# Kernel tuning notes

Measured on AMD Instinct MI355X. Metric: run time of the kernel, lower is better.

The kernel has to match this reference:

```python
import jax, jax.numpy as jnp
import numpy as np

N_NODES = 100000
N_EDGES = 3200000
IN_F = 128
HID = 32


def setup_inputs() -> dict:
    key = jax.random.key(0)
    k = jax.random.split(key, 8)
    x = jax.random.normal(k[0], (N_NODES, IN_F), dtype=jnp.float32)
    edge_index = jax.random.randint(k[1], (2, N_EDGES), 0, N_NODES, dtype=jnp.int64)
    edge_weight = jax.random.uniform(k[2], (N_EDGES,), dtype=jnp.float32)
    # GCN conv weight (in -> 32) and bias, then Linear(32 -> 1)
    s1 = 1.0 / np.sqrt(IN_F)
    s2 = 1.0 / np.sqrt(HID)
    W1 = jax.random.uniform(k[3], (IN_F, HID), dtype=jnp.float32, minval=-s1, maxval=s1)
    b1 = jax.random.uniform(k[4], (HID,), dtype=jnp.float32, minval=-s1, maxval=s1)
    W2 = jax.random.uniform(k[5], (HID, 1), dtype=jnp.float32, minval=-s2, maxval=s2)
    b2 = jax.random.uniform(k[6], (1,), dtype=jnp.float32, minval=-s2, maxval=s2)
    return {"x": x, "edge_index": edge_index, "edge_weight": edge_weight,
            "W1": W1, "b1": b1, "W2": W2, "b2": b2}


def gcn_conv(x, edge_index, edge_weight, W, b):
    N = x.shape[0]
    src = edge_index[0]
    dst = edge_index[1]
    loop = jnp.arange(N, dtype=edge_index.dtype)
    row = jnp.concatenate([dst, loop])  # aggregation targets
    col = jnp.concatenate([src, loop])  # message sources
    w = jnp.concatenate([edge_weight, jnp.ones((N,), dtype=x.dtype)])
    deg = jax.ops.segment_sum(w, row, num_segments=N)
    dinv = jnp.where(deg > 0, deg ** -0.5, 0.0).astype(x.dtype)
    norm = dinv[row] * w * dinv[col]  # [E+N]
    h = x @ W  # [N, 32]  transform before gather (cheaper)
    msgs = norm[:, None] * h[col]  # [E+N, 32]
    agg = jax.ops.segment_sum(msgs, row, num_segments=N)  # [N, 32]
    return agg + b


def reference(x, edge_index, edge_weight, W1, b1, W2, b2):
    h = gcn_conv(x, edge_index, edge_weight, W1, b1)
    h = jax.nn.relu(h)
    return h @ W2 + b2  # [N, 1]
```

## Files before the change

kernel.cpp:

```cpp
#include <hip/hip_runtime.h>
#include <hip/hip_bf16.h>
#include <hip/hip_fp16.h>

#define NN 100000
#define NE 3200000
#define IN_F 128
#define HID 32

#define NB 782
#define NBP1 (NB + 1)
#define BNODES 128
#define PBLK 782
#define EPB 4096
#define SSPAN 4608

typedef __hip_bfloat16 bf16;
typedef __attribute__((ext_vector_type(8))) short s16x8;
typedef __attribute__((ext_vector_type(4))) float f32x4;

__global__ __launch_bounds__(512) void k_part(const int* __restrict__ ei,
                                              const float* __restrict__ ew,
                                              int* __restrict__ offs,
                                              uint2* __restrict__ raw) {
    __shared__ int hist[NB];
    __shared__ int start[NB];
    __shared__ int wtot8[8];
    __shared__ uint2 sp[EPB];

    int t = threadIdx.x;
    int blk = blockIdx.x;
    for (int b = t; b < NB; b += 512) hist[b] = 0;
    __syncthreads();

    unsigned pk[8]; unsigned wb[8]; int bkt[8];
    int base_e = blk * EPB;
#pragma unroll
    for (int j = 0; j < 8; j++) {
        int e = base_e + j * 512 + t;
        if (e < NE) {
            int src = __builtin_nontemporal_load(ei + e);
            int dst = __builtin_nontemporal_load(ei + NE + e);
            float w = __builtin_nontemporal_load(ew + e);
            bkt[j] = dst >> 7;
            pk[j] = (unsigned)src | ((unsigned)(dst & 127) << 20);
            wb[j] = __float_as_uint(w);
        } else bkt[j] = -1;
    }
#pragma unroll
    for (int j = 0; j < 8; j++)
        if (bkt[j] >= 0) atomicAdd(&hist[bkt[j]], 1);
    __syncthreads();

    int e0 = 2 * t, e1 = 2 * t + 1;
    int h0 = (e0 < NB) ? hist[e0] : 0;
    int h1 = (e1 < NB) ? hist[e1] : 0;
    int psum = h0 + h1;
    int lane = t & 63;
    int incl = psum;
#pragma unroll
    for (int off = 1; off < 64; off <<= 1) {
        int up = __shfl_up(incl, off, 64);
        if (lane >= off) incl += up;
    }
    int wid = t >> 6;
    if (lane == 63) wtot8[wid] = incl;
    __syncthreads();
    int woff = 0;
    for (int wj = 0; wj < wid; wj++) woff += wtot8[wj];
    int exc = woff + incl - psum;
    if (e0 < NB) start[e0] = exc;
    if (e1 < NB) start[e1] = exc + h0;
    __syncthreads();

    int total = start[NB - 1] + hist[NB - 1];
    int* orow = offs + (size_t)blk * NBP1;
    for (int b = t; b < NB; b += 512) orow[b] = start[b];
    if (t == 0) orow[NB] = total;
    __syncthreads();

#pragma unroll
    for (int j = 0; j < 8; j++) {
        if (bkt[j] >= 0) {
            int pos = atomicAdd(&start[bkt[j]], 1);
            sp[pos] = make_uint2(pk[j], wb[j]);
        }
    }
    __syncthreads();

    uint2* r = raw + (size_t)blk * EPB;
    for (int i = t; i < total; i += 512) r[i] = sp[i];
}

__global__ __launch_bounds__(256) void k_trans(const int* __restrict__ in, int* __restrict__ out) {
    __shared__ int tile[32][33];
    int c0 = blockIdx.x * 32, r0 = blockIdx.y * 32;
    int tx = threadIdx.x & 31, ty = threadIdx.x >> 5;
    for (int i = ty; i < 32; i += 8) {
        int r = r0 + i, c = c0 + tx;
        if (r < PBLK && c < NBP1) tile[i][tx] = in[(size_t)r * NBP1 + c];
    }
    __syncthreads();
    for (int i = ty; i < 32; i += 8) {
        int c = c0 + i, r = r0 + tx;
        if (c < NBP1 && r < PBLK) out[(size_t)c * PBLK + r] = tile[tx][i];
    }
}

__global__ __launch_bounds__(512) void k_sort(const int* __restrict__ offsT,
                                              const uint2* __restrict__ raw,
                                              uint2* __restrict__ srt,
                                              int* __restrict__ rowstart,
                                              int* __restrict__ rowcnt,
                                              float* __restrict__ dinv) {
    __shared__ uint2 se[SSPAN];
    __shared__ unsigned short runid[SSPAN];
    __shared__ int P[PBLK + 1];
    __shared__ int O0[PBLK];
    __shared__ int hist[BNODES];
    __shared__ float wsum[BNODES];
    __shared__ int scanbuf[BNODES];
    __shared__ int cur[BNODES];
    __shared__ int wt8[8];

    int t = threadIdx.x;
    int b = blockIdx.x;
    if (t < BNODES) { hist[t] = 0; wsum[t] = 1.0f; }

    int e0 = 2 * t, e1 = 2 * t + 1;
    int l0 = 0, l1 = 0, o0v = 0, o1v = 0;
    if (e0 < PBLK) {
        o0v = offsT[(size_t)b * PBLK + e0];
        l0  = offsT[(size_t)(b + 1) * PBLK + e0] - o0v;
    }
    if (e1 < PBLK) {
        o1v = offsT[(size_t)b * PBLK + e1];
        l1  = offsT[(size_t)(b + 1) * PBLK + e1] - o1v;
    }
    int psum = l0 + l1;
    int lane = t & 63;
    int incl = psum;
#pragma unroll
    for (int off = 1; off < 64; off <<= 1) {
        int up = __shfl_up(incl, off, 64);
        if (lane >= off) incl += up;
    }
    int wid = t >> 6;
    if (lane == 63) wt8[wid] = incl;
    __syncthreads();
    int woff = 0;
    for (int wj = 0; wj < wid; wj++) woff += wt8[wj];
    int exc = woff + incl - psum;
    if (e0 < PBLK) { P[e0] = exc;      O0[e0] = o0v; }
    if (e1 < PBLK) { P[e1] = exc + l0; O0[e1] = o1v; }
    if (t == 0) {
        int s = 0;
#pragma unroll
        for (int j = 0; j < 8; j++) s += wt8[j];
        P[PBLK] = s;
    }
    __syncthreads();

    int total = min(P[PBLK], SSPAN);

    for (int r = t; r < PBLK; r += 512) {
        int p0 = P[r], p1 = min(P[r + 1], SSPAN);
        for (int i = p0; i < p1; i++) runid[i] = (unsigned short)r;
    }
    __syncthreads();

    uint2 rr[9];
#pragma unroll
    for (int k = 0; k < 9; k++) {
        int d = t + k * 512;
        if (d < total) {
            int r = runid[d];
            uint2 rec = raw[(size_t)r * EPB + O0[r] + (d - P[r])];
            rr[k] = rec;
            int dl = (rec.x >> 20) & 127;
            atomicAdd(&hist[dl], 1);
            atomicAdd(&wsum[dl], __uint_as_float(rec.y));
        }
    }
    __syncthreads();

    if (t < BNODES) scanbuf[t] = hist[t];
    __syncthreads();
    for (int off = 1; off < BNODES; off <<= 1) {
        int v = 0;
        if (t < BNODES && t >= off) v = scanbuf[t - off];
        __syncthreads();
        if (t < BNODES) scanbuf[t] += v;
        __syncthreads();
    }

    int obase = b * SSPAN;
    if (t < BNODES) {
        int binstart = scanbuf[t] - hist[t];
        cur[t] = binstart;
        int node = b * BNODES + t;
        if (node < NN) {
            rowstart[node] = obase + binstart;
            rowcnt[node]   = hist[t];
            dinv[node]     = rsqrtf(wsum[t]);
        }
    }
    __syncthreads();

#pragma unroll
    for (int k = 0; k < 9; k++) {
        int d = t + k * 512;
        if (d < total) {
            uint2 rec = rr[k];
            int dl = (rec.x >> 20) & 127;
            int pos = atomicAdd(&cur[dl], 1);
            se[pos] = make_uint2(rec.x & 0xFFFFF, rec.y);
        }
    }
    __syncthreads();

    for (int i = t; i < total; i += 512) srt[obase + i] = se[i];
}

__global__ void k_w1frag(const float* __restrict__ W1, unsigned short* __restrict__ wfrag) {
    int lane = threadIdx.x;
    int q = lane >> 4;
    int n0 = lane & 15;
#pragma unroll
    for (int ks = 0; ks < 4; ks++) {
#pragma unroll
        for (int nt = 0; nt < 2; nt++) {
            int fi = ks * 2 + nt;
            int n = n0 + 16 * nt;
#pragma unroll
            for (int j = 0; j < 8; j++) {
                int k = ks * 32 + q * 8 + j;
                float v = W1[k * HID + n];
                __hip_bfloat16 bv = __float2bfloat16(v);
                wfrag[((size_t)fi * 64 + lane) * 8 + j] = *(unsigned short*)&bv;
            }
        }
    }
}

__global__ __launch_bounds__(256) void k_hs(const float* __restrict__ x,
                                            const unsigned short* __restrict__ wfrag,
                                            const float* __restrict__ dinv,
                                            bf16* __restrict__ hs) {
    int t = threadIdx.x;
    int lane = t & 63;
    int wv = t >> 6;
    int base = blockIdx.x * 64 + wv * 16;
    int m = lane & 15;
    int q = lane >> 4;
    int node = base + m;

    s16x8 wf[8];
    const s16x8* wp = (const s16x8*)wfrag;
#pragma unroll
    for (int fi = 0; fi < 8; fi++) wf[fi] = wp[fi * 64 + lane];

    f32x4 acc0 = {0.f, 0.f, 0.f, 0.f};
    f32x4 acc1 = {0.f, 0.f, 0.f, 0.f};

    const float* rowp = x + (size_t)node * IN_F + q * 8;
    bool valid = (node < NN);

#pragma unroll
    for (int ks = 0; ks < 4; ks++) {
        float4 f0 = {0,0,0,0}, f1 = {0,0,0,0};
        if (valid) {
            const float4* xr = (const float4*)(rowp + ks * 32);
            f0 = xr[0]; f1 = xr[1];
        }
        union { s16x8 v; unsigned u32[4]; } af;
        __hip_bfloat162 p0 = __float22bfloat162_rn({f0.x, f0.y});
        __hip_bfloat162 p1 = __float22bfloat162_rn({f0.z, f0.w});
        __hip_bfloat162 p2 = __float22bfloat162_rn({f1.x, f1.y});
        __hip_bfloat162 p3 = __float22bfloat162_rn({f1.z, f1.w});
        af.u32[0] = *(unsigned*)&p0;
        af.u32[1] = *(unsigned*)&p1;
        af.u32[2] = *(unsigned*)&p2;
        af.u32[3] = *(unsigned*)&p3;
        acc0 = __builtin_amdgcn_mfma_f32_16x16x32_bf16(af.v, wf[ks * 2 + 0], acc0, 0, 0, 0);
        acc1 = __builtin_amdgcn_mfma_f32_16x16x32_bf16(af.v, wf[ks * 2 + 1], acc1, 0, 0, 0);
    }

    int f = lane & 15;
#pragma unroll
    for (int r = 0; r < 4; r++) {
        int n2 = base + q * 4 + r;
        if (n2 < NN) {
            float dv = dinv[n2];
            hs[(size_t)n2 * HID + f]      = __float2bfloat16(dv * acc0[r]);
            hs[(size_t)n2 * HID + f + 16] = __float2bfloat16(dv * acc1[r]);
        }
    }
}

__global__ __launch_bounds__(256) void k_agg(const int* __restrict__ rowstart,
                                             const int* __restrict__ rowcnt,
                                             const uint2* __restrict__ eb,
                                             const bf16* __restrict__ hs,
                                             const float* __restrict__ dinv,
                                             const float* __restrict__ b1, const float* __restrict__ W2,
                                             const float* __restrict__ b2, float* __restrict__ out) {
    int t = threadIdx.x;
    int l = t & 15;
    int node = blockIdx.x * 16 + (t >> 4);
    int rs = rowstart[node];
    int re = rs + rowcnt[node];
    const __hip_bfloat162* hs2 = (const __hip_bfloat162*)hs;
    float acc0 = 0.f, acc1 = 0.f;

    for (int base = rs; base < re; base += 16) {
        int idx = base + l;
        int sreg = 0; float wreg = 0.f;
        if (idx < re) {
            uint2 r = eb[idx];
            sreg = (int)r.x;
            wreg = __uint_as_float(r.y);
        }
        int m = min(16, re - base);
        int j = 0;
        for (; j + 8 <= m; j += 8) {
            int s0 = __shfl(sreg, j + 0, 16), s1 = __shfl(sreg, j + 1, 16);
            int s2 = __shfl(sreg, j + 2, 16), s3 = __shfl(sreg, j + 3, 16);
            int s4 = __shfl(sreg, j + 4, 16), s5 = __shfl(sreg, j + 5, 16);
            int s6 = __shfl(sreg, j + 6, 16), s7 = __shfl(sreg, j + 7, 16);
            float w0 = __shfl(wreg, j + 0, 16), w1 = __shfl(wreg, j + 1, 16);
            float w2 = __shfl(wreg, j + 2, 16), w3 = __shfl(wreg, j + 3, 16);
            float w4 = __shfl(wreg, j + 4, 16), w5 = __shfl(wreg, j + 5, 16);
            float w6 = __shfl(wreg, j + 6, 16), w7 = __shfl(wreg, j + 7, 16);
            __hip_bfloat162 h0 = hs2[(size_t)s0 * 16 + l];
            __hip_bfloat162 h1 = hs2[(size_t)s1 * 16 + l];
            __hip_bfloat162 h2 = hs2[(size_t)s2 * 16 + l];
            __hip_bfloat162 h3 = hs2[(size_t)s3 * 16 + l];
            __hip_bfloat162 h4 = hs2[(size_t)s4 * 16 + l];
            __hip_bfloat162 h5 = hs2[(size_t)s5 * 16 + l];
            __hip_bfloat162 h6 = hs2[(size_t)s6 * 16 + l];
            __hip_bfloat162 h7 = hs2[(size_t)s7 * 16 + l];
            float2 f0 = __bfloat1622float2(h0); acc0 += w0 * f0.x; acc1 += w0 * f0.y;
            float2 f1 = __bfloat1622float2(h1); acc0 += w1 * f1.x; acc1 += w1 * f1.y;
            float2 f2 = __bfloat1622float2(h2); acc0 += w2 * f2.x; acc1 += w2 * f2.y;
            float2 f3 = __bfloat1622float2(h3); acc0 += w3 * f3.x; acc1 += w3 * f3.y;
            float2 f4 = __bfloat1622float2(h4); acc0 += w4 * f4.x; acc1 += w4 * f4.y;
            float2 f5 = __bfloat1622float2(h5); acc0 += w5 * f5.x; acc1 += w5 * f5.y;
            float2 f6 = __bfloat1622float2(h6); acc0 += w6 * f6.x; acc1 += w6 * f6.y;
            float2 f7 = __bfloat1622float2(h7); acc0 += w7 * f7.x; acc1 += w7 * f7.y;
        }
        for (; j < m; j++) {
            int s = __shfl(sreg, j, 16);
            float w = __shfl(wreg, j, 16);
            float2 fv = __bfloat1622float2(hs2[(size_t)s * 16 + l]);
            acc0 += w * fv.x; acc1 += w * fv.y;
        }
    }

    float2 fs = __bfloat1622float2(hs2[(size_t)node * 16 + l]);
    float dv = dinv[node];
    float v0 = dv * (acc0 + fs.x) + b1[2 * l];
    float v1 = dv * (acc1 + fs.y) + b1[2 * l + 1];
    v0 = fmaxf(v0, 0.f);
    v1 = fmaxf(v1, 0.f);
    float psum = v0 * W2[2 * l] + v1 * W2[2 * l + 1];
#pragma unroll
    for (int m2 = 8; m2 >= 1; m2 >>= 1) psum += __shfl_xor(psum, m2, 16);
    if (l == 0) out[node] = psum + b2[0];
}

extern "C" void kernel_launch(void* const* d_in, const int* in_sizes, int n_in,
                              void* d_out, int out_size, void* d_ws, size_t ws_size,
                              hipStream_t stream) {
    const float* x  = (const float*)d_in[0];
    const int*   ei = (const int*)d_in[1];
    const float* ew = (const float*)d_in[2];
    const float* W1 = (const float*)d_in[3];
    const float* b1 = (const float*)d_in[4];
    const float* W2 = (const float*)d_in[5];
    const float* b2 = (const float*)d_in[6];
    float* out = (float*)d_out;

    char* ws = (char*)d_ws;
    uint2*          raw      = (uint2*)         (ws + 0);
    bf16*           hs       = (bf16*)          (ws + 0);
    int*            offs     = (int*)           (ws + 25624576);
    int*            offsT    = (int*)           (ws + 28073984);
    uint2*          srt      = (uint2*)         (ws + 30523392);
    int*            rowstart = (int*)           (ws + 59351040);
    int*            rowcnt   = (int*)           (ws + 59751040);
    float*          dinv     = (float*)         (ws + 60151040);
    unsigned short* wfrag    = (unsigned short*)(ws + 60551040);

    k_w1frag<<<1, 64, 0, stream>>>(W1, wfrag);
    k_part<<<PBLK, 512, 0, stream>>>(ei, ew, offs, raw);
    k_trans<<<dim3((NBP1 + 31) / 32, (PBLK + 31) / 32), 256, 0, stream>>>(offs, offsT);
    k_sort<<<NB, 512, 0, stream>>>(offsT, raw, srt, rowstart, rowcnt, dinv);
    k_hs<<<(NN + 63) / 64, 256, 0, stream>>>(x, wfrag, dinv, hs);
    k_agg<<<NN / 16, 256, 0, stream>>>(rowstart, rowcnt, srt, hs, dinv, b1, W2, b2, out);
}
```

Before: 216.6 us.

## Fuse per-bucket sort into aggregation kernel and compute degrees via global fixed-point atomics

Removes the separate sort kernel. The bucket sort now runs in shared memory inside the aggregation kernel, so the sorted edge array no longer goes through global memory. Weighted degrees are accumulated during partitioning with integer atomics on a fixed-point scale into a zeroed global buffer, and dinv is derived in the hs kernel. This costs 3.2M global atomics, a memset, some fixed-point rounding in the degree, and a heavier aggregation kernel where each 16-lane group handles 4 nodes serially, with fewer blocks and lower occupancy.

```diff
diff --git a/kernel.cpp b/kernel.cpp
--- a/kernel.cpp
+++ b/kernel.cpp
@@ -13,6 +13,8 @@
 #define PBLK 782
 #define EPB 4096
 #define SSPAN 4608
+#define WSCALE 16777216.0f
+#define WSCALE_INV 5.9604644775390625e-08f
 
 typedef __hip_bfloat16 bf16;
 typedef __attribute__((ext_vector_type(8))) short s16x8;
@@ -21,7 +23,8 @@
 __global__ __launch_bounds__(512) void k_part(const int* __restrict__ ei,
                                               const float* __restrict__ ew,
                                               int* __restrict__ offs,
-                                              uint2* __restrict__ raw) {
+                                              uint2* __restrict__ raw,
+                                              int* __restrict__ wsumi) {
     __shared__ int hist[NB];
     __shared__ int start[NB];
     __shared__ int wtot8[8];
@@ -48,7 +51,11 @@
     }
 #pragma unroll
     for (int j = 0; j < 8; j++)
-        if (bkt[j] >= 0) atomicAdd(&hist[bkt[j]], 1);
+        if (bkt[j] >= 0) {
+            atomicAdd(&hist[bkt[j]], 1);
+            int dst = (bkt[j] << 7) | (int)((pk[j] >> 20) & 127);
+            atomicAdd(&wsumi[dst], (int)(__uint_as_float(wb[j]) * WSCALE));
+        }
     __syncthreads();
 
     int e0 = 2 * t, e1 = 2 * t + 1;
@@ -106,121 +113,6 @@
     }
 }
 
-__global__ __launch_bounds__(512) void k_sort(const int* __restrict__ offsT,
-                                              const uint2* __restrict__ raw,
-                                              uint2* __restrict__ srt,
-                                              int* __restrict__ rowstart,
-                                              int* __restrict__ rowcnt,
-                                              float* __restrict__ dinv) {
-    __shared__ uint2 se[SSPAN];
-    __shared__ unsigned short runid[SSPAN];
-    __shared__ int P[PBLK + 1];
-    __shared__ int O0[PBLK];
-    __shared__ int hist[BNODES];
-    __shared__ float wsum[BNODES];
-    __shared__ int scanbuf[BNODES];
-    __shared__ int cur[BNODES];
-    __shared__ int wt8[8];
-
-    int t = threadIdx.x;
-    int b = blockIdx.x;
-    if (t < BNODES) { hist[t] = 0; wsum[t] = 1.0f; }
-
-    int e0 = 2 * t, e1 = 2 * t + 1;
-    int l0 = 0, l1 = 0, o0v = 0, o1v = 0;
-    if (e0 < PBLK) {
-        o0v = offsT[(size_t)b * PBLK + e0];
-        l0  = offsT[(size_t)(b + 1) * PBLK + e0] - o0v;
-    }
-    if (e1 < PBLK) {
-        o1v = offsT[(size_t)b * PBLK + e1];
-        l1  = offsT[(size_t)(b + 1) * PBLK + e1] - o1v;
-    }
-    int psum = l0 + l1;
-    int lane = t & 63;
-    int incl = psum;
-#pragma unroll
-    for (int off = 1; off < 64; off <<= 1) {
-        int up = __shfl_up(incl, off, 64);
-        if (lane >= off) incl += up;
-    }
-    int wid = t >> 6;
-    if (lane == 63) wt8[wid] = incl;
-    __syncthreads();
-    int woff = 0;
-    for (int wj = 0; wj < wid; wj++) woff += wt8[wj];
-    int exc = woff + incl - psum;
-    if (e0 < PBLK) { P[e0] = exc;      O0[e0] = o0v; }
-    if (e1 < PBLK) { P[e1] = exc + l0; O0[e1] = o1v; }
-    if (t == 0) {
-        int s = 0;
-#pragma unroll
-        for (int j = 0; j < 8; j++) s += wt8[j];
-        P[PBLK] = s;
-    }
-    __syncthreads();
-
-    int total = min(P[PBLK], SSPAN);
-
-    for (int r = t; r < PBLK; r += 512) {
-        int p0 = P[r], p1 = min(P[r + 1], SSPAN);
-        for (int i = p0; i < p1; i++) runid[i] = (unsigned short)r;
-    }
-    __syncthreads();
-
-    uint2 rr[9];
-#pragma unroll
-    for (int k = 0; k < 9; k++) {
-        int d = t + k * 512;
-        if (d < total) {
-            int r = runid[d];
-            uint2 rec = raw[(size_t)r * EPB + O0[r] + (d - P[r])];
-            rr[k] = rec;
-            int dl = (rec.x >> 20) & 127;
-            atomicAdd(&hist[dl], 1);
-            atomicAdd(&wsum[dl], __uint_as_float(rec.y));
-        }
-    }
-    __syncthreads();
-
-    if (t < BNODES) scanbuf[t] = hist[t];
-    __syncthreads();
-    for (int off = 1; off < BNODES; off <<= 1) {
-        int v = 0;
-        if (t < BNODES && t >= off) v = scanbuf[t - off];
-        __syncthreads();
-        if (t < BNODES) scanbuf[t] += v;
-        __syncthreads();
-    }
-
-    int obase = b * SSPAN;
-    if (t < BNODES) {
-        int binstart = scanbuf[t] - hist[t];
-        cur[t] = binstart;
-        int node = b * BNODES + t;
-        if (node < NN) {
-            rowstart[node] = obase + binstart;
-            rowcnt[node]   = hist[t];
-            dinv[node]     = rsqrtf(wsum[t]);
-        }
-    }
-    __syncthreads();
-
-#pragma unroll
-    for (int k = 0; k < 9; k++) {
-        int d = t + k * 512;
-        if (d < total) {
-            uint2 rec = rr[k];
-            int dl = (rec.x >> 20) & 127;
-            int pos = atomicAdd(&cur[dl], 1);
-            se[pos] = make_uint2(rec.x & 0xFFFFF, rec.y);
-        }
-    }
-    __syncthreads();
-
-    for (int i = t; i < total; i += 512) srt[obase + i] = se[i];
-}
-
 __global__ void k_w1frag(const float* __restrict__ W1, unsigned short* __restrict__ wfrag) {
     int lane = threadIdx.x;
     int q = lane >> 4;
@@ -244,7 +136,8 @@
 
 __global__ __launch_bounds__(256) void k_hs(const float* __restrict__ x,
                                             const unsigned short* __restrict__ wfrag,
-                                            const float* __restrict__ dinv,
+                                            const int* __restrict__ wsumi,
+                                            float* __restrict__ dinv,
                                             bf16* __restrict__ hs) {
     int t = threadIdx.x;
     int lane = t & 63;
@@ -290,82 +183,172 @@
     for (int r = 0; r < 4; r++) {
         int n2 = base + q * 4 + r;
         if (n2 < NN) {
-            float dv = dinv[n2];
+            float dv = rsqrtf((float)wsumi[n2] * WSCALE_INV + 1.0f);
+            if (f == 0) dinv[n2] = dv;
             hs[(size_t)n2 * HID + f]      = __float2bfloat16(dv * acc0[r]);
             hs[(size_t)n2 * HID + f + 16] = __float2bfloat16(dv * acc1[r]);
         }
     }
 }
 
-__global__ __launch_bounds__(256) void k_agg(const int* __restrict__ rowstart,
-                                             const int* __restrict__ rowcnt,
-                                             const uint2* __restrict__ eb,
+__global__ __launch_bounds__(512) void k_agg(const int* __restrict__ offsT,
+                                             const uint2* __restrict__ raw,
                                              const bf16* __restrict__ hs,
                                              const float* __restrict__ dinv,
                                              const float* __restrict__ b1, const float* __restrict__ W2,
                                              const float* __restrict__ b2, float* __restrict__ out) {
+    __shared__ uint2 se[SSPAN];
+    __shared__ int P[PBLK + 1];
+    __shared__ int basearr[PBLK];
+    __shared__ int hist[BNODES];
+    __shared__ int scanbuf[BNODES];
+    __shared__ int cur[BNODES];
+    __shared__ int wt8[8];
+
+    unsigned short* runid = (unsigned short*)se;
+
     int t = threadIdx.x;
+    int b = blockIdx.x;
+    if (t < BNODES) hist[t] = 0;
+
+    int e0 = 2 * t, e1 = 2 * t + 1;
+    int l0 = 0, l1 = 0, o0v = 0, o1v = 0;
+    if (e0 < PBLK) {
+        o0v = offsT[(size_t)b * PBLK + e0];
+        l0  = offsT[(size_t)(b + 1) * PBLK + e0] - o0v;
+    }
+    if (e1 < PBLK) {
+        o1v = offsT[(size_t)b * PBLK + e1];
+        l1  = offsT[(size_t)(b + 1) * PBLK + e1] - o1v;
+    }
+    int psum = l0 + l1;
+    int lane = t & 63;
+    int incl = psum;
+#pragma unroll
+    for (int off = 1; off < 64; off <<= 1) {
+        int up = __shfl_up(incl, off, 64);
+        if (lane >= off) incl += up;
+    }
+    int wid = t >> 6;
+    if (lane == 63) wt8[wid] = incl;
+    __syncthreads();
+    int woff = 0;
+    for (int wj = 0; wj < wid; wj++) woff += wt8[wj];
+    int exc = woff + incl - psum;
+    if (e0 < PBLK) { P[e0] = exc;      basearr[e0] = o0v - exc; }
+    if (e1 < PBLK) { P[e1] = exc + l0; basearr[e1] = o1v - (exc + l0); }
+    if (t == 0) {
+        int s = 0;
+#pragma unroll
+        for (int j = 0; j < 8; j++) s += wt8[j];
+        P[PBLK] = s;
+    }
+    __syncthreads();
+
+    int total = min(P[PBLK], SSPAN);
+
+    for (int r = t; r < PBLK; r += 512) {
+        int p0 = P[r], p1 = min(P[r + 1], SSPAN);
+        for (int i = p0; i < p1; i++) runid[i] = (unsigned short)r;
+    }
+    __syncthreads();
+
+    uint2 rr[9];
+#pragma unroll
+    for (int k = 0; k < 9; k++) {
+        int d = t + k * 512;
+        if (d < total) {
+            int r = runid[d];
+            uint2 rec = raw[(size_t)r * EPB + (basearr[r] + d)];
+            rr[k] = rec;
+            int dl = (rec.x >> 20) & 127;
+            atomicAdd(&hist[dl], 1);
+        }
+    }
+    __syncthreads();
+
+    if (t < BNODES) scanbuf[t] = hist[t];
+    __syncthreads();
+    for (int off = 1; off < BNODES; off <<= 1) {
+        int v = 0;
+        if (t < BNODES && t >= off) v = scanbuf[t - off];
+        __syncthreads();
+        if (t < BNODES) scanbuf[t] += v;
+        __syncthreads();
+    }
+    if (t < BNODES) cur[t] = scanbuf[t] - hist[t];
+    __syncthreads();
+
+#pragma unroll
+    for (int k = 0; k < 9; k++) {
+        int d = t + k * 512;
+        if (d < total) {
+            uint2 rec = rr[k];
+            int dl = (rec.x >> 20) & 127;
+            int pos = atomicAdd(&cur[dl], 1);
+            se[pos] = make_uint2(rec.x & 0xFFFFF, rec.y);
+        }
+    }
+    __syncthreads();
+
+    int gid = t >> 4;
     int l = t & 15;
-    int node = blockIdx.x * 16 + (t >> 4);
-    int rs = rowstart[node];
-    int re = rs + rowcnt[node];
     const __hip_bfloat162* hs2 = (const __hip_bfloat162*)hs;
-    float acc0 = 0.f, acc1 = 0.f;
-
-    for (int base = rs; base < re; base += 16) {
-        int idx = base + l;
-        int sreg = 0; float wreg = 0.f;
-        if (idx < re) {
-            uint2 r = eb[idx];
-            sreg = (int)r.x;
-            wreg = __uint_as_float(r.y);
-        }
-        int m = min(16, re - base);
-        int j = 0;
-        for (; j + 8 <= m; j += 8) {
-            int s0 = __shfl(sreg, j + 0, 16), s1 = __shfl(sreg, j + 1, 16);
-            int s2 = __shfl(sreg, j + 2, 16), s3 = __shfl(sreg, j + 3, 16);
-            int s4 = __shfl(sreg, j + 4, 16), s5 = __shfl(sreg, j + 5, 16);
-            int s6 = __shfl(sreg, j + 6, 16), s7 = __shfl(sreg, j + 7, 16);
-            float w0 = __shfl(wreg, j + 0, 16), w1 = __shfl(wreg, j + 1, 16);
-            float w2 = __shfl(wreg, j + 2, 16), w3 = __shfl(wreg, j + 3, 16);
-            float w4 = __shfl(wreg, j + 4, 16), w5 = __shfl(wreg, j + 5, 16);
-            float w6 = __shfl(wreg, j + 6, 16), w7 = __shfl(wreg, j + 7, 16);
-            __hip_bfloat162 h0 = hs2[(size_t)s0 * 16 + l];
-            __hip_bfloat162 h1 = hs2[(size_t)s1 * 16 + l];
-            __hip_bfloat162 h2 = hs2[(size_t)s2 * 16 + l];
-            __hip_bfloat162 h3 = hs2[(size_t)s3 * 16 + l];
-            __hip_bfloat162 h4 = hs2[(size_t)s4 * 16 + l];
-            __hip_bfloat162 h5 = hs2[(size_t)s5 * 16 + l];
-            __hip_bfloat162 h6 = hs2[(size_t)s6 * 16 + l];
-            __hip_bfloat162 h7 = hs2[(size_t)s7 * 16 + l];
-            float2 f0 = __bfloat1622float2(h0); acc0 += w0 * f0.x; acc1 += w0 * f0.y;
-            float2 f1 = __bfloat1622float2(h1); acc0 += w1 * f1.x; acc1 += w1 * f1.y;
-            float2 f2 = __bfloat1622float2(h2); acc0 += w2 * f2.x; acc1 += w2 * f2.y;
-            float2 f3 = __bfloat1622float2(h3); acc0 += w3 * f3.x; acc1 += w3 * f3.y;
-            float2 f4 = __bfloat1622float2(h4); acc0 += w4 * f4.x; acc1 += w4 * f4.y;
-            float2 f5 = __bfloat1622float2(h5); acc0 += w5 * f5.x; acc1 += w5 * f5.y;
-            float2 f6 = __bfloat1622float2(h6); acc0 += w6 * f6.x; acc1 += w6 * f6.y;
-            float2 f7 = __bfloat1622float2(h7); acc0 += w7 * f7.x; acc1 += w7 * f7.y;
-        }
-        for (; j < m; j++) {
-            int s = __shfl(sreg, j, 16);
-            float w = __shfl(wreg, j, 16);
-            float2 fv = __bfloat1622float2(hs2[(size_t)s * 16 + l]);
-            acc0 += w * fv.x; acc1 += w * fv.y;
-        }
-    }
-
-    float2 fs = __bfloat1622float2(hs2[(size_t)node * 16 + l]);
-    float dv = dinv[node];
-    float v0 = dv * (acc0 + fs.x) + b1[2 * l];
-    float v1 = dv * (acc1 + fs.y) + b1[2 * l + 1];
-    v0 = fmaxf(v0, 0.f);
-    v1 = fmaxf(v1, 0.f);
-    float psum = v0 * W2[2 * l] + v1 * W2[2 * l + 1];
-#pragma unroll
-    for (int m2 = 8; m2 >= 1; m2 >>= 1) psum += __shfl_xor(psum, m2, 16);
-    if (l == 0) out[node] = psum + b2[0];
+#pragma unroll
+    for (int nn = 0; nn < 4; nn++) {
+        int dl = gid * 4 + nn;
+        int cnt = hist[dl];
+        int rs = scanbuf[dl] - cnt;
+        float a0 = 0.f, a1 = 0.f;
+        for (int bse = 0; bse < cnt; bse += 8) {
+            int rem = cnt - bse;
+            uint2 q0 = se[rs + bse];
+            uint2 q1 = se[rs + bse + (rem > 1 ? 1 : 0)];
+            uint2 q2 = se[rs + bse + (rem > 2 ? 2 : 0)];
+            uint2 q3 = se[rs + bse + (rem > 3 ? 3 : 0)];
+            uint2 q4 = se[rs + bse + (rem > 4 ? 4 : 0)];
+            uint2 q5 = se[rs + bse + (rem > 5 ? 5 : 0)];
+            uint2 q6 = se[rs + bse + (rem > 6 ? 6 : 0)];
+            uint2 q7 = se[rs + bse + (rem > 7 ? 7 : 0)];
+            float w0 = __uint_as_float(q0.y);
+            float w1 = rem > 1 ? __uint_as_float(q1.y) : 0.f;
+            float w2 = rem > 2 ? __uint_as_float(q2.y) : 0.f;
+            float w3 = rem > 3 ? __uint_as_float(q3.y) : 0.f;
+            float w4 = rem > 4 ? __uint_as_float(q4.y) : 0.f;
+            float w5 = rem > 5 ? __uint_as_float(q5.y) : 0.f;
+            float w6 = rem > 6 ? __uint_as_float(q6.y) : 0.f;
+            float w7 = rem > 7 ? __uint_as_float(q7.y) : 0.f;
+            __hip_bfloat162 h0 = hs2[(size_t)q0.x * 16 + l];
+            __hip_bfloat162 h1 = hs2[(size_t)q1.x * 16 + l];
+            __hip_bfloat162 h2 = hs2[(size_t)q2.x * 16 + l];
+            __hip_bfloat162 h3 = hs2[(size_t)q3.x * 16 + l];
+            __hip_bfloat162 h4 = hs2[(size_t)q4.x * 16 + l];
+            __hip_bfloat162 h5 = hs2[(size_t)q5.x * 16 + l];
+            __hip_bfloat162 h6 = hs2[(size_t)q6.x * 16 + l];
+            __hip_bfloat162 h7 = hs2[(size_t)q7.x * 16 + l];
+            float2 f0 = __bfloat1622float2(h0); a0 += w0 * f0.x; a1 += w0 * f0.y;
+            float2 f1 = __bfloat1622float2(h1); a0 += w1 * f1.x; a1 += w1 * f1.y;
+            float2 f2 = __bfloat1622float2(h2); a0 += w2 * f2.x; a1 += w2 * f2.y;
+            float2 f3 = __bfloat1622float2(h3); a0 += w3 * f3.x; a1 += w3 * f3.y;
+            float2 f4 = __bfloat1622float2(h4); a0 += w4 * f4.x; a1 += w4 * f4.y;
+            float2 f5 = __bfloat1622float2(h5); a0 += w5 * f5.x; a1 += w5 * f5.y;
+            float2 f6 = __bfloat1622float2(h6); a0 += w6 * f6.x; a1 += w6 * f6.y;
+            float2 f7 = __bfloat1622float2(h7); a0 += w7 * f7.x; a1 += w7 * f7.y;
+        }
+        int node = b * BNODES + dl;
+        if (node < NN) {
+            float dv = dinv[node];
+            float2 fs = __bfloat1622float2(hs2[(size_t)node * 16 + l]);
+            float v0 = dv * (a0 + fs.x) + b1[2 * l];
+            float v1 = dv * (a1 + fs.y) + b1[2 * l + 1];
+            v0 = fmaxf(v0, 0.f);
+            v1 = fmaxf(v1, 0.f);
+            float ps = v0 * W2[2 * l] + v1 * W2[2 * l + 1];
+#pragma unroll
+            for (int m2 = 8; m2 >= 1; m2 >>= 1) ps += __shfl_xor(ps, m2, 16);
+            if (l == 0) out[node] = ps + b2[0];
+        }
+    }
 }
 
 extern "C" void kernel_launch(void* const* d_in, const int* in_sizes, int n_in,
@@ -382,19 +365,17 @@
 
     char* ws = (char*)d_ws;
     uint2*          raw      = (uint2*)         (ws + 0);
-    bf16*           hs       = (bf16*)          (ws + 0);
     int*            offs     = (int*)           (ws + 25624576);
     int*            offsT    = (int*)           (ws + 28073984);
-    uint2*          srt      = (uint2*)         (ws + 30523392);
-    int*            rowstart = (int*)           (ws + 59351040);
-    int*            rowcnt   = (int*)           (ws + 59751040);
-    float*          dinv     = (float*)         (ws + 60151040);
-    unsigned short* wfrag    = (unsigned short*)(ws + 60551040);
-
+    bf16*           hs       = (bf16*)          (ws + 30523392);
+    int*            wsumi    = (int*)           (ws + 36923392);
+    float*          dinv     = (float*)         (ws + 37323392);
+    unsigned short* wfrag    = (unsigned short*)(ws + 37723392);
+
+    (void)hipMemsetAsync(wsumi, 0, NN * sizeof(int), stream);
     k_w1frag<<<1, 64, 0, stream>>>(W1, wfrag);
-    k_part<<<PBLK, 512, 0, stream>>>(ei, ew, offs, raw);
+    k_part<<<PBLK, 512, 0, stream>>>(ei, ew, offs, raw, wsumi);
     k_trans<<<dim3((NBP1 + 31) / 32, (PBLK + 31) / 32), 256, 0, stream>>>(offs, offsT);
-    k_sort<<<NB, 512, 0, stream>>>(offsT, raw, srt, rowstart, rowcnt, dinv);
-    k_hs<<<(NN + 63) / 64, 256, 0, stream>>>(x, wfrag, dinv, hs);
-    k_agg<<<NN / 16, 256, 0, stream>>>(rowstart, rowcnt, srt, hs, dinv, b1, W2, b2, out);
-}
+    k_hs<<<(NN + 63) / 64, 256, 0, stream>>>(x, wfrag, wsumi, dinv, hs);
+    k_agg<<<NB, 512, 0, stream>>>(offsT, raw, hs, dinv, b1, W2, b2, out);
+}
```

New measurement: 322.2 us. +48.8%, slower.
